# Kernel optimization log

Measured on AMD Instinct MI355X. Metric: run time of the kernel, lower is better.

## Reference

```python
import jax, jax.numpy as jnp
import numpy as np

jax.config.update("jax_enable_x64", True)

N = 100000          # occupied voxels
C = 64              # channels
K = 27              # 3x3x3 kernel volume
GRID = 80           # voxel grid extent
SHARED_FXP_SHIFT = 23
SHIFT0 = 31         # SharedFxpShift + requant_shift for input requant
SHIFT1 = 31         # SharedFxpShift + requant_shift after conv1+PReLU
PRELU_SHIFT = 25    # PReLU slope fixed-point shift (slope = round(a * 2^25))
ACT_RANGE = 127


def _build_neighbor_maps(rng):
    # sample N unique occupied voxels in an 80^3 grid
    flat = rng.choice(GRID ** 3, size=N, replace=False)
    x = flat // (GRID * GRID)
    y = (flat // GRID) % GRID
    z = flat % GRID
    G2 = GRID + 2  # pad by 1 so shifted coords stay in-range
    lut = -np.ones(G2 * G2 * G2, dtype=np.int64)
    lut[(x + 1) * G2 * G2 + (y + 1) * G2 + (z + 1)] = np.arange(N)
    offs = [(dx, dy, dz) for dx in (-1, 0, 1) for dy in (-1, 0, 1) for dz in (-1, 0, 1)]
    in_idx = np.empty((N, K), dtype=np.int64)
    for k, (dx, dy, dz) in enumerate(offs):
        in_idx[:, k] = lut[(x + dx + 1) * G2 * G2 + (y + dy + 1) * G2 + (z + dz + 1)]
    mask = in_idx >= 0
    in_idx = np.where(mask, in_idx, 0)
    return in_idx.astype(np.int32), mask


def setup_inputs() -> dict:
    rng = np.random.default_rng(0)
    in_idx, mask = _build_neighbor_maps(rng)
    x32 = rng.integers(-20000, 20000, size=(N, C)).astype(np.int32)
    w1 = rng.integers(-127, 128, size=(K, C, C)).astype(np.int8)   # [k, out, in]
    w2 = rng.integers(-127, 128, size=(K, C, C)).astype(np.int8)
    b1 = rng.integers(-1000, 1000, size=(C,)).astype(np.int32)
    b2 = rng.integers(-1000, 1000, size=(C,)).astype(np.int32)
    comp1 = rng.integers(-500, 500, size=(K, C)).astype(np.int32)  # zero-point compensation
    comp2 = rng.integers(-500, 500, size=(K, C)).astype(np.int32)
    mul1 = rng.integers(1000000, 1200000, size=(C,)).astype(np.int64)  # per-channel requant_mul (uint32 range)
    return {
        "x32": jnp.asarray(x32),
        "in_idx": jnp.asarray(in_idx),
        "mask": jnp.asarray(mask),
        "w1": jnp.asarray(w1), "b1": jnp.asarray(b1), "comp1": jnp.asarray(comp1),
        "w2": jnp.asarray(w2), "b2": jnp.asarray(b2), "comp2": jnp.asarray(comp2),
        "mul0": jnp.asarray(13675000, dtype=jnp.int64),
        "mul1": jnp.asarray(mul1),
        "slope": jnp.asarray(6710886, dtype=jnp.int64),  # round(0.2 * 2^25)
    }


def _requant_to_int8(x, mul, total_shift):
    # RequantFxpToScaledInt8: fixed-point multiply, arithmetic shift, clip to int8 range
    v = (x.astype(jnp.int64) * mul) >> total_shift
    return jnp.clip(v, -ACT_RANGE, ACT_RANGE).astype(jnp.int8)


def _sparse_conv_in8w8out32(f8, w, b, comp, in_idx, mask):
    # per-offset gather-GEMM-scatter, expressed as one masked gather + batched int8 GEMM
    g = jnp.where(mask[:, :, None], f8[in_idx], jnp.int8(0))           # [N, K, Cin] int8
    acc = jnp.einsum("nki,koi->no", g, w, preferred_element_type=jnp.int32)  # int32 accum
    # zero-point compensation added once per valid (offset, out) pair, plus bias
    acc = acc + mask.astype(jnp.int32) @ comp + b[None, :]
    return acc


def _prelu_int32(x, slope):
    x64 = x.astype(jnp.int64)
    return jnp.where(x64 >= 0, x64, (x64 * slope) >> PRELU_SHIFT)


def reference(x32, in_idx, mask, w1, b1, comp1, w2, b2, comp2, mul0, mul1, slope):
    q0 = _requant_to_int8(x32, mul0, SHIFT0)                 # int32 -> int8
    a1 = _sparse_conv_in8w8out32(q0, w1, b1, comp1, in_idx, mask)  # int32
    p1 = _prelu_int32(a1, slope)                             # int64 fixed-point PReLU
    q1 = _requant_to_int8(p1, mul1[None, :], SHIFT1)         # per-channel requant -> int8
    a2 = _sparse_conv_in8w8out32(q1, w2, b2, comp2, in_idx, mask)  # int32
    return a2 + x32                                          # int32 residual add
```

## Files before the change

### kernel.cpp

```cpp
#include <hip/hip_runtime.h>
#include <stdint.h>

#define CCH 64
#define KK 27
#define WN (KK * CCH * CCH)

typedef int v4i __attribute__((ext_vector_type(4)));

__global__ void __launch_bounds__(256) k_prep(
    const int* __restrict__ x32, const int* __restrict__ mul0p,
    const int* __restrict__ w1_32, const int* __restrict__ w2_32,
    const int* __restrict__ comp1, const int* __restrict__ b1,
    const int* __restrict__ comp2, const int* __restrict__ b2,
    int8_t* __restrict__ w1e, int8_t* __restrict__ w2e,
    int* __restrict__ q0, int* __restrict__ zpage,
    int prep_blocks, int total4)
{
    const int bid = blockIdx.x;
    if (bid < prep_blocks) {
        const int gtid = bid * 256 + threadIdx.x;
        if (gtid < WN) {
            w1e[gtid] = (int8_t)w1_32[gtid];
        } else if (gtid < 2 * WN) {
            w2e[gtid - WN] = (int8_t)w2_32[gtid - WN];
        } else if (gtid < 2 * WN + 8192) {
            int u = gtid - 2 * WN;
            const int which = u >> 12;
            u &= 4095;
            const int col = u >> 6, j = u & 63;
            const int* comp = which ? comp2 : comp1;
            const int* bias = which ? b2 : b1;
            int v;
            if (j < 27)       v = comp[j * CCH + col] >> 2;
            else if (j < 54)  v = comp[(j - 27) * CCH + col] & 3;
            else if (j == 54) v = bias[col] >> 6;
            else if (j == 55) v = bias[col] & 63;
            else              v = 0;
            (which ? w2e : w1e)[27 * 4096 + col * 64 + j] = (int8_t)v;
        } else {
            const int u = gtid - 2 * WN - 8192;
            if (u < 64) zpage[u] = 0;
        }
    } else {
        const int i = (bid - prep_blocks) * 256 + threadIdx.x;
        if (i < total4) {
            const int mul2 = (*mul0p) << 1;
            const int4 v = ((const int4*)x32)[i];
            int r = 0, q;
            q = __mulhi(v.x, mul2); q = q > 127 ? 127 : (q < -127 ? -127 : q); r |= (q & 0xff);
            q = __mulhi(v.y, mul2); q = q > 127 ? 127 : (q < -127 ? -127 : q); r |= (q & 0xff) << 8;
            q = __mulhi(v.z, mul2); q = q > 127 ? 127 : (q < -127 ? -127 : q); r |= (q & 0xff) << 16;
            q = __mulhi(v.w, mul2); q = q > 127 ? 127 : (q < -127 ? -127 : q); r |= (q & 0xff) << 24;
            q0[i] = r;
        }
    }
}

__device__ __forceinline__ v4i affine_frag(const int* __restrict__ idxm,
                                           int row, int q) {
    v4i r;
#pragma unroll
    for (int d = 0; d < 4; ++d) {
        int pk = 0;
#pragma unroll
        for (int b = 0; b < 4; ++b) {
            const int ch = q * 16 + d * 4 + b;
            int cc = (ch < 27) ? ch : ch - 27;
            cc = (cc > 26) ? 0 : cc;
            const int m = (idxm[row * KK + cc] >= 0) ? 1 : 0;
            const int bv = (ch < 27) ? (m << 2)
                         : (ch < 54) ? m
                         : (ch == 54) ? 64
                         : (ch == 55) ? 1 : 0;
            pk |= bv << (8 * b);
        }
        r[d] = pk;
    }
    return r;
}

template <int LAYER>
__global__ void __launch_bounds__(256, 2)
k_conv(const int8_t* __restrict__ fin,
       const int* __restrict__ in_idx,
       const int* __restrict__ mask,
       const int8_t* __restrict__ wext,
       const int* __restrict__ mul1,
       const int* __restrict__ slopep,
       const int* __restrict__ x32,
       const int8_t* __restrict__ zpage,
       int8_t* __restrict__ q1out,
       int* __restrict__ out,
       int ntiles)
{
    __shared__ int s_idxm[2][16 * KK];
    __shared__ v4i s_red[2][4][4][64];

    const int tid  = threadIdx.x;
    const int lane = tid & 63;
    const int wv   = tid >> 6;
    const int arow = lane & 15;
    const int srow = lane >> 4;
    const int col  = wv * 16 + arow;
    const int e0 = tid;
    const int e1 = tid + 176;

    v4i wreg[7][4];
#pragma unroll
    for (int j = 0; j < 7; ++j)
#pragma unroll
        for (int g = 0; g < 4; ++g)
            wreg[j][g] = *(const v4i*)(wext +
                ((size_t)((7 * wv + j) * CCH + g * 16 + arow)) * CCH + srow * 16);

    const int mul2     = (LAYER == 1) ? (mul1[col] << 1) : 0;
    const int slope128 = (LAYER == 1) ? ((*slopep) << 7) : 0;

    const int stride = gridDim.x;
    const int t0 = blockIdx.x;
    if (t0 >= ntiles) return;
    const int cnt = (ntiles - 1 - t0) / stride + 1;

    v4i aA[7], aB[7];
    v4i accP = {0, 0, 0, 0};

#define GATHER_A(AN, SN)                                                       \
    _Pragma("unroll")                                                          \
    for (int j = 0; j < 7; ++j) {                                              \
        if (wv == 3 && j == 6) {                                               \
            AN[6] = affine_frag(&s_idxm[SN][0], arow, srow);                   \
        } else {                                                               \
            const int v_ = s_idxm[SN][arow * KK + (7 * wv + j)];               \
            const int8_t* src_ = (v_ >= 0)                                     \
                ? (fin + (size_t)v_ * CCH + srow * 16)                         \
                : (zpage + srow * 16);                                         \
            AN[j] = *(const v4i*)src_;                                         \
        }                                                                      \
    }

#define EPILOGUE(TOT, NBP, X0, X1, X2, X3)                                     \
    if (LAYER == 1) {                                                          \
        _Pragma("unroll")                                                      \
        for (int r = 0; r < 4; ++r) {                                          \
            const int v_ = TOT[r];                                             \
            const int p_ = (v_ >= 0) ? v_ : __mulhi(v_, slope128);             \
            int q_ = __mulhi(p_, mul2);                                        \
            q_ = q_ > 127 ? 127 : (q_ < -127 ? -127 : q_);                     \
            q1out[(size_t)((NBP) + srow * 4 + r) * CCH + col] = (int8_t)q_;    \
        }                                                                      \
    } else {                                                                   \
        out[(size_t)((NBP) + srow * 4 + 0) * CCH + col] = TOT[0] + X0;         \
        out[(size_t)((NBP) + srow * 4 + 1) * CCH + col] = TOT[1] + X1;         \
        out[(size_t)((NBP) + srow * 4 + 2) * CCH + col] = TOT[2] + X2;         \
        out[(size_t)((NBP) + srow * 4 + 3) * CCH + col] = TOT[3] + X3;         \
    }

#define ITER(AC, AN, P, DO_EPI)                                                \
    do {                                                                       \
             \
        int tp2_ = t + 2 * stride; if (tp2_ >= ntiles) tp2_ = ntiles - 1;      \
        const size_t b2_ = (size_t)tp2_ * (16 * KK);                           \
        const int qa0_ = in_idx[b2_ + e0], qm0_ = mask[b2_ + e0];              \
        const int qa1_ = in_idx[b2_ + e1], qm1_ = mask[b2_ + e1];              \
        const int nbp_ = (t - stride) * 16;                                    \
        int xr0_ = 0, xr1_ = 0, xr2_ = 0, xr3_ = 0;                            \
        if (DO_EPI && LAYER == 2) {                                            \
            xr0_ = x32[(size_t)(nbp_ + srow * 4 + 0) * CCH + col];             \
            xr1_ = x32[(size_t)(nbp_ + srow * 4 + 1) * CCH + col];             \
            xr2_ = x32[(size_t)(nbp_ + srow * 4 + 2) * CCH + col];             \
            xr3_ = x32[(size_t)(nbp_ + srow * 4 + 3) * CCH + col];             \
        }                                                                      \
                                          \
        GATHER_A(AN, (P) ^ 1)                                                  \
        __builtin_amdgcn_sched_barrier(0);                                     \
                                                       \
        v4i acc0 = {0,0,0,0}, acc1 = {0,0,0,0}, acc2 = {0,0,0,0}, acc3 = {0,0,0,0}; \
        _Pragma("unroll")                                                      \
        for (int j = 0; j < 7; ++j) {                                          \
            acc0 = __builtin_amdgcn_mfma_i32_16x16x64_i8(AC[j], wreg[j][0], acc0, 0, 0, 0); \
            acc1 = __builtin_amdgcn_mfma_i32_16x16x64_i8(AC[j], wreg[j][1], acc1, 0, 0, 0); \
            acc2 = __builtin_amdgcn_mfma_i32_16x16x64_i8(AC[j], wreg[j][2], acc2, 0, 0, 0); \
            acc3 = __builtin_amdgcn_mfma_i32_16x16x64_i8(AC[j], wreg[j][3], acc3, 0, 0, 0); \
        }                                                                      \
                      \
        if (wv != 0) s_red[P][wv][0][lane] = acc0;                             \
        if (wv != 1) s_red[P][wv][1][lane] = acc1;                             \
        if (wv != 2) s_red[P][wv][2][lane] = acc2;                             \
        if (wv != 3) s_red[P][wv][3][lane] = acc3;                             \
                       \
        if (DO_EPI) {                                                          \
            v4i tot = accP;                                                    \
            _Pragma("unroll")                                                  \
            for (int w = 0; w < 4; ++w) {                                      \
                if (w != wv) {                                                 \
                    const v4i r_ = s_red[(P) ^ 1][w][wv][lane];                \
                    tot[0] += r_[0]; tot[1] += r_[1];                          \
                    tot[2] += r_[2]; tot[3] += r_[3];                          \
                }                                                              \
            }                                                                  \
            EPILOGUE(tot, nbp_, xr0_, xr1_, xr2_, xr3_)                        \
        }                                                                      \
                        \
        s_idxm[P][e0] = qm0_ ? qa0_ : -1;                                      \
        s_idxm[P][e1] = qm1_ ? qa1_ : -1;                                      \
        accP = (wv == 0) ? acc0 : (wv == 1) ? acc1 : (wv == 2) ? acc2 : acc3;  \
        asm volatile("s_waitcnt lgkmcnt(0)" ::: "memory");                     \
        __builtin_amdgcn_s_barrier();                                          \
    } while (0)

    int pa0, pa1, pm0, pm1;
    {
        const size_t base = (size_t)t0 * (16 * KK);
        const int a0 = in_idx[base + e0], m0 = mask[base + e0];
        const int a1 = in_idx[base + e1], m1 = mask[base + e1];
        s_idxm[0][e0] = m0 ? a0 : -1;
        s_idxm[0][e1] = m1 ? a1 : -1;
    }
    {
        int t1c = t0 + stride; if (t1c >= ntiles) t1c = ntiles - 1;
        const size_t base = (size_t)t1c * (16 * KK);
        pa0 = in_idx[base + e0]; pm0 = mask[base + e0];
        pa1 = in_idx[base + e1]; pm1 = mask[base + e1];
    }
    __syncthreads();
    GATHER_A(aA, 0)
    s_idxm[1][e0] = pm0 ? pa0 : -1;
    s_idxm[1][e1] = pm1 ? pa1 : -1;
    asm volatile("s_waitcnt lgkmcnt(0)" ::: "memory");
    __builtin_amdgcn_s_barrier();

    int t = t0;
    ITER(aA, aB, 0, 0);
    t += stride;
    int i = 1;
    while (i < cnt) {
        ITER(aB, aA, 1, 1);
        ++i; t += stride; if (i >= cnt) break;
        ITER(aA, aB, 0, 1);
        ++i; t += stride;
    }

    {
        const int pl = (cnt - 1) & 1;
        const int nbl = (t0 + (cnt - 1) * stride) * 16;
        int x0 = 0, x1 = 0, x2 = 0, x3 = 0;
        if (LAYER == 2) {
            x0 = x32[(size_t)(nbl + srow * 4 + 0) * CCH + col];
            x1 = x32[(size_t)(nbl + srow * 4 + 1) * CCH + col];
            x2 = x32[(size_t)(nbl + srow * 4 + 2) * CCH + col];
            x3 = x32[(size_t)(nbl + srow * 4 + 3) * CCH + col];
        }
        v4i tot = accP;
#pragma unroll
        for (int w = 0; w < 4; ++w) {
            if (w != wv) {
                const v4i r_ = s_red[pl][w][wv][lane];
                tot[0] += r_[0]; tot[1] += r_[1];
                tot[2] += r_[2]; tot[3] += r_[3];
            }
        }
        EPILOGUE(tot, nbl, x0, x1, x2, x3)
    }
#undef ITER
#undef EPILOGUE
#undef GATHER_A
}

extern "C" void kernel_launch(void* const* d_in, const int* in_sizes, int n_in,
                              void* d_out, int out_size, void* d_ws, size_t ws_size,
                              hipStream_t stream) {
    const int* x32    = (const int*)d_in[0];
    const int* in_idx = (const int*)d_in[1];
    const int* mask   = (const int*)d_in[2];
    const int* w1_32  = (const int*)d_in[3];
    const int* b1     = (const int*)d_in[4];
    const int* comp1  = (const int*)d_in[5];
    const int* w2_32  = (const int*)d_in[6];
    const int* b2     = (const int*)d_in[7];
    const int* comp2  = (const int*)d_in[8];
    const int* mul0   = (const int*)d_in[9];
    const int* mul1   = (const int*)d_in[10];
    const int* slope  = (const int*)d_in[11];

    const int nvox = in_sizes[0] / CCH;
    const size_t wext_b = (size_t)28 * CCH * CCH;
    const size_t fbytes = (size_t)nvox * CCH;
    const size_t falign = (fbytes + 255) & ~(size_t)255;
    const size_t walign = (wext_b + 255) & ~(size_t)255;

    int8_t* q0;
    int8_t* q1;
    int8_t* w1e;
    int8_t* w2e;
    if (ws_size >= 2 * falign + 2 * walign + 256) {
        q0  = (int8_t*)d_ws;
        q1  = q0 + falign;
        w1e = q1 + falign;
        w2e = w1e + walign;
    } else {
        q0  = (int8_t*)d_out;
        q1  = (int8_t*)d_ws;
        w1e = q1 + falign;
        w2e = w1e + walign;
    }
    int8_t* zpage = w2e + walign;

    const int total4 = (nvox * CCH) / 4;
    const int prep_blocks = (2 * WN + 8192 + 64 + 255) / 256;
    const int req_blocks  = (total4 + 255) / 256;
    k_prep<<<prep_blocks + req_blocks, 256, 0, stream>>>(
        x32, mul0, w1_32, w2_32, comp1, b1, comp2, b2,
        w1e, w2e, (int*)q0, (int*)zpage, prep_blocks, total4);

    const int ntiles = nvox / 16;
    int cblocks = 512;
    if (cblocks > ntiles) cblocks = ntiles;
    k_conv<1><<<cblocks, 256, 0, stream>>>(q0, in_idx, mask, w1e,
                                           mul1, slope, nullptr, zpage,
                                           q1, nullptr, ntiles);
    k_conv<2><<<cblocks, 256, 0, stream>>>(q1, in_idx, mask, w2e,
                                           nullptr, nullptr, x32, zpage,
                                           nullptr, (int*)d_out, ntiles);
}
```

Measured before the change: 65.51 us.

## Precompute mask-affine fragments in prep kernel and use sentinel zero row offsets

Moves the per-tile construction of the affine (compensation/bias) A-fragment out of the conv inner loop into the prep kernel, which writes a 64-byte per-voxel fragment buffer that both convs load directly. Shared-memory neighbor indices are stored as precomputed byte offsets, with missing neighbors pointing to an appended zero row in each feature buffer, removing the select-against-zpage branch. This cuts ALU and LDS reads from the hot loop at the cost of an extra prep pass reading the mask and an extra 6.4MB buffer read per conv.

After: 56.27 us. 1.16x faster.

```diff
diff --git a/kernel.cpp b/kernel.cpp
--- a/kernel.cpp
+++ b/kernel.cpp
@@ -12,12 +12,13 @@
     const int* __restrict__ w1_32, const int* __restrict__ w2_32,
     const int* __restrict__ comp1, const int* __restrict__ b1,
     const int* __restrict__ comp2, const int* __restrict__ b2,
+    const int* __restrict__ mask,
     int8_t* __restrict__ w1e, int8_t* __restrict__ w2e,
-    int* __restrict__ q0, int* __restrict__ zpage,
-    int prep_blocks, int total4)
+    int* __restrict__ q0, int* __restrict__ q1, int8_t* __restrict__ af,
+    int pb1, int af_blocks, int nvox, int total4)
 {
     const int bid = blockIdx.x;
-    if (bid < prep_blocks) {
+    if (bid < pb1) {
         const int gtid = bid * 256 + threadIdx.x;
         if (gtid < WN) {
             w1e[gtid] = (int8_t)w1_32[gtid];
@@ -39,10 +40,40 @@
             (which ? w2e : w1e)[27 * 4096 + col * 64 + j] = (int8_t)v;
         } else {
             const int u = gtid - 2 * WN - 8192;
-            if (u < 64) zpage[u] = 0;
+            if (u < 16)       q0[(size_t)nvox * 16 + u] = 0;
+            else if (u < 32)  q1[(size_t)nvox * 16 + (u - 16)] = 0;
+        }
+    } else if (bid < pb1 + af_blocks) {
+        const int vox = (bid - pb1) * 256 + threadIdx.x;
+        if (vox < nvox) {
+            int m[27];
+#pragma unroll
+            for (int k = 0; k < 27; ++k)
+                m[k] = mask[(size_t)vox * 27 + k] ? 1 : 0;
+            v4i d0, d1, d2, d3;
+#pragma unroll
+            for (int di = 0; di < 16; ++di) {
+                int pk = 0;
+#pragma unroll
+                for (int b = 0; b < 4; ++b) {
+                    const int ch = di * 4 + b;
+                    int bv = 0;
+                    if (ch < 27)       bv = m[ch] << 2;
+                    else if (ch < 54)  bv = m[ch - 27];
+                    else if (ch == 54) bv = 64;
+                    else if (ch == 55) bv = 1;
+                    pk |= bv << (8 * b);
+                }
+                if (di < 4)       d0[di] = pk;
+                else if (di < 8)  d1[di - 4] = pk;
+                else if (di < 12) d2[di - 8] = pk;
+                else              d3[di - 12] = pk;
+            }
+            v4i* dst = (v4i*)(af + (size_t)vox * 64);
+            dst[0] = d0; dst[1] = d1; dst[2] = d2; dst[3] = d3;
         }
     } else {
-        const int i = (bid - prep_blocks) * 256 + threadIdx.x;
+        const int i = (bid - pb1 - af_blocks) * 256 + threadIdx.x;
         if (i < total4) {
             const int mul2 = (*mul0p) << 1;
             const int4 v = ((const int4*)x32)[i];
@@ -56,44 +87,21 @@
     }
 }
 
-__device__ __forceinline__ v4i affine_frag(const int* __restrict__ idxm,
-                                           int row, int q) {
-    v4i r;
-#pragma unroll
-    for (int d = 0; d < 4; ++d) {
-        int pk = 0;
-#pragma unroll
-        for (int b = 0; b < 4; ++b) {
-            const int ch = q * 16 + d * 4 + b;
-            int cc = (ch < 27) ? ch : ch - 27;
-            cc = (cc > 26) ? 0 : cc;
-            const int m = (idxm[row * KK + cc] >= 0) ? 1 : 0;
-            const int bv = (ch < 27) ? (m << 2)
-                         : (ch < 54) ? m
-                         : (ch == 54) ? 64
-                         : (ch == 55) ? 1 : 0;
-            pk |= bv << (8 * b);
-        }
-        r[d] = pk;
-    }
-    return r;
-}
-
 template <int LAYER>
 __global__ void __launch_bounds__(256, 2)
 k_conv(const int8_t* __restrict__ fin,
        const int* __restrict__ in_idx,
        const int* __restrict__ mask,
        const int8_t* __restrict__ wext,
+       const int8_t* __restrict__ af,
        const int* __restrict__ mul1,
        const int* __restrict__ slopep,
        const int* __restrict__ x32,
-       const int8_t* __restrict__ zpage,
        int8_t* __restrict__ q1out,
        int* __restrict__ out,
-       int ntiles)
+       int nvox, int ntiles)
 {
-    __shared__ int s_idxm[2][16 * KK];
+    __shared__ int s_off[2][16 * KK];
     __shared__ v4i s_red[2][4][4][64];
 
     const int tid  = threadIdx.x;
@@ -124,40 +132,39 @@
     v4i aA[7], aB[7];
     v4i accP = {0, 0, 0, 0};
 
-#define GATHER_A(AN, SN)                                                       \
+#define GATHER_A(AN, SN, NB)                                                   \
     _Pragma("unroll")                                                          \
     for (int j = 0; j < 7; ++j) {                                              \
         if (wv == 3 && j == 6) {                                               \
-            AN[6] = affine_frag(&s_idxm[SN][0], arow, srow);                   \
+            AN[6] = *(const v4i*)(af + (size_t)((NB) + arow) * CCH + srow * 16); \
         } else {                                                               \
-            const int v_ = s_idxm[SN][arow * KK + (7 * wv + j)];               \
-            const int8_t* src_ = (v_ >= 0)                                     \
-                ? (fin + (size_t)v_ * CCH + srow * 16)                         \
-                : (zpage + srow * 16);                                         \
-            AN[j] = *(const v4i*)src_;                                         \
+            const int off_ = s_off[SN][arow * KK + (7 * wv + j)];              \
+            AN[j] = *(const v4i*)(fin + off_ + srow * 16);                     \
         }                                                                      \
     }
 
 #define EPILOGUE(TOT, NBP, X0, X1, X2, X3)                                     \
     if (LAYER == 1) {                                                          \
+        int8_t* rp_ = q1out + (size_t)((NBP) + srow * 4) * CCH + col;          \
         _Pragma("unroll")                                                      \
         for (int r = 0; r < 4; ++r) {                                          \
             const int v_ = TOT[r];                                             \
             const int p_ = (v_ >= 0) ? v_ : __mulhi(v_, slope128);             \
             int q_ = __mulhi(p_, mul2);                                        \
             q_ = q_ > 127 ? 127 : (q_ < -127 ? -127 : q_);                     \
-            q1out[(size_t)((NBP) + srow * 4 + r) * CCH + col] = (int8_t)q_;    \
+            rp_[r * CCH] = (int8_t)q_;                                         \
         }                                                                      \
     } else {                                                                   \
-        out[(size_t)((NBP) + srow * 4 + 0) * CCH + col] = TOT[0] + X0;         \
-        out[(size_t)((NBP) + srow * 4 + 1) * CCH + col] = TOT[1] + X1;         \
-        out[(size_t)((NBP) + srow * 4 + 2) * CCH + col] = TOT[2] + X2;         \
-        out[(size_t)((NBP) + srow * 4 + 3) * CCH + col] = TOT[3] + X3;         \
+        int* rp_ = out + (size_t)((NBP) + srow * 4) * CCH + col;               \
+        rp_[0 * CCH] = TOT[0] + X0;                                            \
+        rp_[1 * CCH] = TOT[1] + X1;                                            \
+        rp_[2 * CCH] = TOT[2] + X2;                                            \
+        rp_[3 * CCH] = TOT[3] + X3;                                            \
     }
 
 #define ITER(AC, AN, P, DO_EPI)                                                \
     do {                                                                       \
-             \
+                      \
         int tp2_ = t + 2 * stride; if (tp2_ >= ntiles) tp2_ = ntiles - 1;      \
         const size_t b2_ = (size_t)tp2_ * (16 * KK);                           \
         const int qa0_ = in_idx[b2_ + e0], qm0_ = mask[b2_ + e0];              \
@@ -165,13 +172,12 @@
         const int nbp_ = (t - stride) * 16;                                    \
         int xr0_ = 0, xr1_ = 0, xr2_ = 0, xr3_ = 0;                            \
         if (DO_EPI && LAYER == 2) {                                            \
-            xr0_ = x32[(size_t)(nbp_ + srow * 4 + 0) * CCH + col];             \
-            xr1_ = x32[(size_t)(nbp_ + srow * 4 + 1) * CCH + col];             \
-            xr2_ = x32[(size_t)(nbp_ + srow * 4 + 2) * CCH + col];             \
-            xr3_ = x32[(size_t)(nbp_ + srow * 4 + 3) * CCH + col];             \
+            const int* xp_ = x32 + (size_t)(nbp_ + srow * 4) * CCH + col;      \
+            xr0_ = xp_[0 * CCH]; xr1_ = xp_[1 * CCH];                          \
+            xr2_ = xp_[2 * CCH]; xr3_ = xp_[3 * CCH];                          \
         }                                                                      \
                                           \
-        GATHER_A(AN, (P) ^ 1)                                                  \
+        GATHER_A(AN, (P) ^ 1, (t + stride < ntiles ? (t + stride) * 16 : (ntiles - 1) * 16)) \
         __builtin_amdgcn_sched_barrier(0);                                     \
                                                        \
         v4i acc0 = {0,0,0,0}, acc1 = {0,0,0,0}, acc2 = {0,0,0,0}, acc3 = {0,0,0,0}; \
@@ -200,9 +206,9 @@
             }                                                                  \
             EPILOGUE(tot, nbp_, xr0_, xr1_, xr2_, xr3_)                        \
         }                                                                      \
-                        \
-        s_idxm[P][e0] = qm0_ ? qa0_ : -1;                                      \
-        s_idxm[P][e1] = qm1_ ? qa1_ : -1;                                      \
+                         \
+        s_off[P][e0] = (qm0_ ? qa0_ : nvox) << 6;                              \
+        s_off[P][e1] = (qm1_ ? qa1_ : nvox) << 6;                              \
         accP = (wv == 0) ? acc0 : (wv == 1) ? acc1 : (wv == 2) ? acc2 : acc3;  \
         asm volatile("s_waitcnt lgkmcnt(0)" ::: "memory");                     \
         __builtin_amdgcn_s_barrier();                                          \
@@ -213,8 +219,8 @@
         const size_t base = (size_t)t0 * (16 * KK);
         const int a0 = in_idx[base + e0], m0 = mask[base + e0];
         const int a1 = in_idx[base + e1], m1 = mask[base + e1];
-        s_idxm[0][e0] = m0 ? a0 : -1;
-        s_idxm[0][e1] = m1 ? a1 : -1;
+        s_off[0][e0] = (m0 ? a0 : nvox) << 6;
+        s_off[0][e1] = (m1 ? a1 : nvox) << 6;
     }
     {
         int t1c = t0 + stride; if (t1c >= ntiles) t1c = ntiles - 1;
@@ -223,9 +229,9 @@
         pa1 = in_idx[base + e1]; pm1 = mask[base + e1];
     }
     __syncthreads();
-    GATHER_A(aA, 0)
-    s_idxm[1][e0] = pm0 ? pa0 : -1;
-    s_idxm[1][e1] = pm1 ? pa1 : -1;
+    GATHER_A(aA, 0, t0 * 16)
+    s_off[1][e0] = (pm0 ? pa0 : nvox) << 6;
+    s_off[1][e1] = (pm1 ? pa1 : nvox) << 6;
     asm volatile("s_waitcnt lgkmcnt(0)" ::: "memory");
     __builtin_amdgcn_s_barrier();
 
@@ -245,10 +251,9 @@
         const int nbl = (t0 + (cnt - 1) * stride) * 16;
         int x0 = 0, x1 = 0, x2 = 0, x3 = 0;
         if (LAYER == 2) {
-            x0 = x32[(size_t)(nbl + srow * 4 + 0) * CCH + col];
-            x1 = x32[(size_t)(nbl + srow * 4 + 1) * CCH + col];
-            x2 = x32[(size_t)(nbl + srow * 4 + 2) * CCH + col];
-            x3 = x32[(size_t)(nbl + srow * 4 + 3) * CCH + col];
+            const int* xp_ = x32 + (size_t)(nbl + srow * 4) * CCH + col;
+            x0 = xp_[0 * CCH]; x1 = xp_[1 * CCH];
+            x2 = xp_[2 * CCH]; x3 = xp_[3 * CCH];
         }
         v4i tot = accP;
 #pragma unroll
@@ -284,7 +289,7 @@
 
     const int nvox = in_sizes[0] / CCH;
     const size_t wext_b = (size_t)28 * CCH * CCH;
-    const size_t fbytes = (size_t)nvox * CCH;
+    const size_t fbytes = (size_t)(nvox + 1) * CCH;
     const size_t falign = (fbytes + 255) & ~(size_t)255;
     const size_t walign = (wext_b + 255) & ~(size_t)255;
 
@@ -292,33 +297,36 @@
     int8_t* q1;
     int8_t* w1e;
     int8_t* w2e;
-    if (ws_size >= 2 * falign + 2 * walign + 256) {
+    int8_t* af;
+    if (ws_size >= 3 * falign + 2 * walign) {
         q0  = (int8_t*)d_ws;
         q1  = q0 + falign;
         w1e = q1 + falign;
         w2e = w1e + walign;
+        af  = w2e + walign;
     } else {
         q0  = (int8_t*)d_out;
         q1  = (int8_t*)d_ws;
         w1e = q1 + falign;
         w2e = w1e + walign;
-    }
-    int8_t* zpage = w2e + walign;
+        af  = w2e + walign;
+    }
 
     const int total4 = (nvox * CCH) / 4;
-    const int prep_blocks = (2 * WN + 8192 + 64 + 255) / 256;
-    const int req_blocks  = (total4 + 255) / 256;
-    k_prep<<<prep_blocks + req_blocks, 256, 0, stream>>>(
-        x32, mul0, w1_32, w2_32, comp1, b1, comp2, b2,
-        w1e, w2e, (int*)q0, (int*)zpage, prep_blocks, total4);
+    const int pb1 = (2 * WN + 8192 + 32 + 255) / 256;
+    const int af_blocks  = (nvox + 255) / 256;
+    const int req_blocks = (total4 + 255) / 256;
+    k_prep<<<pb1 + af_blocks + req_blocks, 256, 0, stream>>>(
+        x32, mul0, w1_32, w2_32, comp1, b1, comp2, b2, mask,
+        w1e, w2e, (int*)q0, (int*)q1, af, pb1, af_blocks, nvox, total4);
 
     const int ntiles = nvox / 16;
     int cblocks = 512;
     if (cblocks > ntiles) cblocks = ntiles;
-    k_conv<1><<<cblocks, 256, 0, stream>>>(q0, in_idx, mask, w1e,
-                                           mul1, slope, nullptr, zpage,
-                                           q1, nullptr, ntiles);
-    k_conv<2><<<cblocks, 256, 0, stream>>>(q1, in_idx, mask, w2e,
-                                           nullptr, nullptr, x32, zpage,
-                                           nullptr, (int*)d_out, ntiles);
+    k_conv<1><<<cblocks, 256, 0, stream>>>(q0, in_idx, mask, w1e, af,
+                                           mul1, slope, nullptr,
+                                           q1, nullptr, nvox, ntiles);
+    k_conv<2><<<cblocks, 256, 0, stream>>>(q1, in_idx, mask, w2e, af,
+                                           nullptr, nullptr, x32,
+                                           nullptr, (int*)d_out, nvox, ntiles);
 }
```
